# Kernel tuning notes

Hardware: AMD Instinct MI355X
Metric: run time of the kernel (lower is better)

## Reference

```python
import jax, jax.numpy as jnp
import numpy as np

B_, N, C, NH, NW = 2048, 64, 512, 16, 64  # N == window_size

def setup_inputs() -> dict:
    key = jax.random.key(0)
    k0, k1, k2, k3 = jax.random.split(key, 4)
    std = 0.02
    return {
        "inputs": jax.random.normal(k0, (B_, N, C), jnp.float32),
        "mask": jnp.zeros((NW, N, N), jnp.float32),  # (0 / -inf) additive window mask
        "qkv_w": jax.random.normal(k1, (3 * C, C), jnp.float32) * std,
        "qkv_b": jnp.zeros((3 * C,), jnp.float32),
        "proj_w": jax.random.normal(k2, (C, C), jnp.float32) * std,
        "proj_b": jnp.zeros((C,), jnp.float32),
        "bias_table": jax.random.normal(k3, (2 * N - 1, NH), jnp.float32) * std,
    }

def reference(inputs, mask, qkv_w, qkv_b, proj_w, proj_b, bias_table):
    b, n, c = inputs.shape
    nh = bias_table.shape[1]
    hd = c // nh
    scale = hd ** -0.5
    # qkv projection -> (3, B_, nh, N, hd)
    qkv = (inputs @ qkv_w.T + qkv_b).reshape(b, n, 3, nh, hd).transpose(2, 0, 3, 1, 4)
    q, k, v = qkv[0] * scale, qkv[1], qkv[2]
    attn = jnp.einsum('bhqd,bhkd->bhqk', q, k)  # (B_, nh, N, N)
    # 1D relative position bias, gathered from table
    rel_idx = jnp.arange(n)[:, None] - jnp.arange(n)[None, :] + (n - 1)  # (N, N)
    rel_bias = bias_table[rel_idx]                 # (N, N, nh)
    attn = attn + rel_bias.transpose(2, 0, 1)[None]  # add (nh, N, N)
    # additive window mask
    nw = mask.shape[0]
    attn = attn.reshape(b // nw, nw, nh, n, n) + mask[None, :, None]
    attn = jax.nn.softmax(attn.reshape(b, nh, n, n), axis=-1)
    out = jnp.einsum('bhqk,bhkd->bqhd', attn, v).reshape(b, n, c)
    return out @ proj_w.T + proj_b
```

## Files before the change

kernel.cpp:

```cpp
#include <hip/hip_runtime.h>

typedef __bf16 bf16x8 __attribute__((ext_vector_type(8)));
typedef float f32x4 __attribute__((ext_vector_type(4)));

__device__ __forceinline__ unsigned short f2bf(float x) {
  union { float f; unsigned int u; } c; c.f = x;
  unsigned int r = c.u + 0x7FFFu + ((c.u >> 16) & 1u);
  return (unsigned short)(r >> 16);
}

__global__ __launch_bounds__(256) void f32_to_bf16_vec4(
    const float* __restrict__ in, unsigned short* __restrict__ out, int n4) {
  int i = blockIdx.x * blockDim.x + threadIdx.x;
  int stride = gridDim.x * blockDim.x;
  const float4* in4 = (const float4*)in;
  ushort4* out4 = (ushort4*)out;
  for (; i < n4; i += stride) {
    float4 f = in4[i];
    ushort4 u;
    u.x = f2bf(f.x); u.y = f2bf(f.y); u.z = f2bf(f.z); u.w = f2bf(f.w);
    out4[i] = u;
  }
}

__global__ __launch_bounds__(256) void build_bias_mask(
    const float* __restrict__ bias_table,
    const float* __restrict__ mask,
    float* __restrict__ M) {
  const int idx = blockIdx.x * 256 + threadIdx.x;
  const int k = idx & 63, q = (idx >> 6) & 63, h = (idx >> 12) & 15, w = idx >> 16;
  M[idx] = bias_table[(q - k + 63) * 16 + h] + mask[(w * 64 + q) * 64 + k];
}

#define GLOAD_LDS16(gp, lp)                                                          \
  __builtin_amdgcn_global_load_lds(                                                  \
      (const __attribute__((address_space(1))) unsigned int*)(uintptr_t)(gp),        \
      (__attribute__((address_space(3))) unsigned int*)(uintptr_t)(lp), 16, 0, 0)

template <int NBN, int EPI>
__global__ __launch_bounds__(512, 2) void gemm256(
    const unsigned short* __restrict__ A,
    const unsigned short* __restrict__ B,
    const float* __restrict__ bias,
    void* __restrict__ C0, void* __restrict__ C1, void* __restrict__ C2,
    int ldc) {
  constexpr int K = 512;
  constexpr int NT = K / 64;
  __shared__ __attribute__((aligned(128))) char lds[131072];

  const int t = threadIdx.x;
  const int lane = t & 63;
  const int wid = t >> 6;
  const int wr = wid >> 2, wc = wid & 3;
  const int lr = lane & 15, lg = lane >> 4;

  const int nwg = gridDim.x;
  const int cpx = nwg >> 3;
  const int wgid = (blockIdx.x & 7) * cpx + (blockIdx.x >> 3);
  const int bm = wgid / NBN, bn = wgid % NBN;
  const int m0 = bm * 256, n0 = bn * 256;

  const char* Ab = (const char*)(A + (size_t)m0 * K);
  const char* Bb = (const char*)(B + (size_t)n0 * K);

  const int r3 = t >> 3, ps = t & 7;

  unsigned aoff[2][2], boff[2][2], adst[2][2], bdst[2][2];
#pragma unroll
  for (int j = 0; j < 2; ++j)
#pragma unroll
    for (int i = 0; i < 2; ++i) {
      const int rowA = i * 128 + j * 64 + r3;
      aoff[j][i] = (unsigned)((rowA * K + ((ps ^ (rowA & 7)) << 3)) * 2);
      adst[j][i] = (unsigned)(rowA * 128 + ps * 16);
      const int rowB = i * 128 + ((r3 >> 5) << 6) + j * 32 + (r3 & 31);
      boff[j][i] = (unsigned)((rowB * K + ((ps ^ (rowB & 7)) << 3)) * 2);
      bdst[j][i] = (unsigned)(65536 + rowB * 128 + ps * 16);
    }

#define STAGE_A(j, tt, buf)                                                   \
  do {                                                                        \
    GLOAD_LDS16(Ab + aoff[j][0] + (tt)*128, lds + (buf)*32768 + adst[j][0]);  \
    GLOAD_LDS16(Ab + aoff[j][1] + (tt)*128, lds + (buf)*32768 + adst[j][1]);  \
  } while (0)
#define STAGE_B(j, tt, buf)                                                   \
  do {                                                                        \
    GLOAD_LDS16(Bb + boff[j][0] + (tt)*128, lds + (buf)*32768 + bdst[j][0]);  \
    GLOAD_LDS16(Bb + boff[j][1] + (tt)*128, lds + (buf)*32768 + bdst[j][1]);  \
  } while (0)

  unsigned abase[2], bbase[2];
#pragma unroll
  for (int kk = 0; kk < 2; ++kk) {
    abase[kk] = (unsigned)((wr * 128 + lr) * 128 + (((kk * 4 + lg) ^ (lr & 7)) << 4));
    bbase[kk] = (unsigned)(65536 + (wc * 64 + lr) * 128 + (((kk * 4 + lg) ^ (lr & 7)) << 4));
  }

  f32x4 acc[8][4];
#pragma unroll
  for (int i = 0; i < 8; ++i)
#pragma unroll
    for (int j = 0; j < 4; ++j) acc[i][j] = f32x4{0.f, 0.f, 0.f, 0.f};

#define PHASE(QM, QN, BUF, STAGE_STMT, TAIL_STMT)                                            \
  do {                                                                                       \
    bf16x8 af[4][2], bfr[2][2];                                                              \
    _Pragma("unroll") for (int mt = 0; mt < 4; ++mt)                                         \
      _Pragma("unroll") for (int kk = 0; kk < 2; ++kk)                                       \
        af[mt][kk] = *(const bf16x8*)(lds + (BUF)*32768 + abase[kk] + (QM)*8192 + mt * 2048);\
    _Pragma("unroll") for (int nt = 0; nt < 2; ++nt)                                         \
      _Pragma("unroll") for (int kk = 0; kk < 2; ++kk)                                       \
        bfr[nt][kk] = *(const bf16x8*)(lds + (BUF)*32768 + bbase[kk] + (QN)*4096 + nt * 2048);\
    STAGE_STMT;                                                                              \
    __builtin_amdgcn_s_barrier();                                                            \
    asm volatile("s_waitcnt lgkmcnt(0)" ::: "memory");                                       \
    __builtin_amdgcn_sched_barrier(0);                                                       \
    __builtin_amdgcn_s_setprio(1);                                                           \
    _Pragma("unroll") for (int mt = 0; mt < 4; ++mt)                                         \
      _Pragma("unroll") for (int nt = 0; nt < 2; ++nt)                                       \
        _Pragma("unroll") for (int kk = 0; kk < 2; ++kk)                                     \
          acc[(QM)*4 + mt][(QN)*2 + nt] = __builtin_amdgcn_mfma_f32_16x16x32_bf16(           \
              af[mt][kk], bfr[nt][kk], acc[(QM)*4 + mt][(QN)*2 + nt], 0, 0, 0);              \
    __builtin_amdgcn_s_setprio(0);                                                           \
    TAIL_STMT;                                                                               \
    __builtin_amdgcn_s_barrier();                                                            \
  } while (0)

  STAGE_A(0, 0, 0); STAGE_B(0, 0, 0); STAGE_A(1, 0, 0); STAGE_B(1, 0, 0);
  STAGE_B(0, 1, 1); STAGE_A(1, 1, 1);
  asm volatile("s_waitcnt vmcnt(4)" ::: "memory");
  __builtin_amdgcn_s_barrier();

#pragma unroll
  for (int tt = 0; tt < NT; ++tt) {
    const int b = tt & 1;
    const int b1 = b ^ 1;
    PHASE(0, 0, b, if (tt + 1 < NT) STAGE_A(0, tt + 1, b1), (void)0);
    PHASE(1, 0, b, if (tt + 1 < NT) STAGE_B(1, tt + 1, b1), (void)0);
    PHASE(1, 1, b, if (tt + 2 < NT) STAGE_B(0, tt + 2, b), (void)0);
    if (tt + 2 < NT) {
      PHASE(0, 1, b, STAGE_A(1, tt + 2, b),
            asm volatile("s_waitcnt vmcnt(4)" ::: "memory"));
    } else if (tt + 1 < NT) {
      PHASE(0, 1, b, (void)0, asm volatile("s_waitcnt vmcnt(0)" ::: "memory"));
    } else {
      PHASE(0, 1, b, (void)0, (void)0);
    }
  }
#undef PHASE
#undef STAGE_A
#undef STAGE_B

#pragma unroll
  for (int qm = 0; qm < 2; ++qm)
#pragma unroll
    for (int mt = 0; mt < 4; ++mt)
#pragma unroll
      for (int qn = 0; qn < 2; ++qn)
#pragma unroll
        for (int nt = 0; nt < 2; ++nt) {
          const int n = n0 + wc * 64 + qn * 32 + nt * 16 + lr;
          const float bv = bias[n];
          const f32x4 a4 = acc[qm * 4 + mt][qn * 2 + nt];
          if constexpr (EPI == 2) {
            const int part = n >> 9;
            unsigned short* dst = part == 0 ? (unsigned short*)C0
                                 : (part == 1 ? (unsigned short*)C1 : (unsigned short*)C2);
            const float sc = (part == 0) ? 0.17677669529663687f : 1.0f;
            const int hh = (n >> 5) & 15, dd = n & 31;
#pragma unroll
            for (int r = 0; r < 4; ++r) {
              const int m = m0 + wr * 128 + qm * 64 + mt * 16 + lg * 4 + r;
              dst[((size_t)((m >> 6) * 16 + hh) * 64 + (m & 63)) * 32 + dd] =
                  f2bf((a4[r] + bv) * sc);
            }
          } else {
#pragma unroll
            for (int r = 0; r < 4; ++r) {
              const int m = m0 + wr * 128 + qm * 64 + mt * 16 + lg * 4 + r;
              ((float*)C0)[(size_t)m * ldc + n] = a4[r] + bv;
            }
          }
        }
}

__global__ __launch_bounds__(128) void attn_kernel(
    const unsigned short* __restrict__ Qh,
    const unsigned short* __restrict__ Kh,
    const unsigned short* __restrict__ Vh,
    const float* __restrict__ M,
    unsigned short* __restrict__ attn_out
) {
  const int wv = threadIdx.x >> 6;
  const int bh = blockIdx.x * 2 + wv;
  const int b = bh >> 4, h = bh & 15;
  const int lane = threadIdx.x & 63;
  const int lr = lane & 15, lg = lane >> 4;

  __shared__ unsigned short VtS[2][32 * 72];
  __shared__ unsigned short PlS[2][16 * 72];
  unsigned short* Vt = VtS[wv];
  unsigned short* Pl = PlS[wv];

  const unsigned short* qb = Qh + (size_t)bh * 2048;
  const unsigned short* kb = Kh + (size_t)bh * 2048;
  const unsigned short* vg = Vh + (size_t)bh * 2048;

  bf16x8 vr[4];
#pragma unroll
  for (int i = 0; i < 4; ++i) vr[i] = ((const bf16x8*)(vg + lane * 32))[i];
  bf16x8 kf[4], qf[4];
#pragma unroll
  for (int nt = 0; nt < 4; ++nt)
    kf[nt] = *(const bf16x8*)(kb + (nt * 16 + lr) * 32 + lg * 8);
#pragma unroll
  for (int mt = 0; mt < 4; ++mt)
    qf[mt] = *(const bf16x8*)(qb + (mt * 16 + lr) * 32 + lg * 8);

  {
    __bf16* vt = (__bf16*)Vt;
#pragma unroll
    for (int d = 0; d < 8; ++d) {
      vt[(d)*72 + lane] = vr[0][d];
      vt[(d + 8) * 72 + lane] = vr[1][d];
      vt[(d + 16) * 72 + lane] = vr[2][d];
      vt[(d + 24) * 72 + lane] = vr[3][d];
    }
  }
  bf16x8 vfrag[2][2];
#pragma unroll
  for (int dt = 0; dt < 2; ++dt)
#pragma unroll
    for (int ki = 0; ki < 2; ++ki)
      vfrag[dt][ki] = *(const bf16x8*)(Vt + (dt * 16 + lr) * 72 + ki * 32 + lg * 8);

  const float* Mb = M + (size_t)((b & 63) * 16 + h) * 4096;

  f32x4 o[4][2];
#pragma unroll
  for (int i = 0; i < 4; ++i)
#pragma unroll
    for (int j = 0; j < 2; ++j) o[i][j] = f32x4{0.f, 0.f, 0.f, 0.f};
  float rinv[4][4];

#pragma unroll
  for (int mt = 0; mt < 4; ++mt) {
    float mv[4][4];
#pragma unroll
    for (int r = 0; r < 4; ++r)
#pragma unroll
      for (int nt = 0; nt < 4; ++nt)
        mv[r][nt] = Mb[(mt * 16 + lg * 4 + r) * 64 + nt * 16 + lr];

    f32x4 s[4];
#pragma unroll
    for (int nt = 0; nt < 4; ++nt) s[nt] = f32x4{0.f, 0.f, 0.f, 0.f};
#pragma unroll
    for (int nt = 0; nt < 4; ++nt)
      s[nt] = __builtin_amdgcn_mfma_f32_16x16x32_bf16(qf[mt], kf[nt], s[nt], 0, 0, 0);

#pragma unroll
    for (int r = 0; r < 4; ++r) {
      float v[4];
#pragma unroll
      for (int nt = 0; nt < 4; ++nt) v[nt] = s[nt][r] + mv[r][nt];
      float mx = fmaxf(fmaxf(v[0], v[1]), fmaxf(v[2], v[3]));
      mx = fmaxf(mx, __shfl_xor(mx, 1, 64));
      mx = fmaxf(mx, __shfl_xor(mx, 2, 64));
      mx = fmaxf(mx, __shfl_xor(mx, 4, 64));
      mx = fmaxf(mx, __shfl_xor(mx, 8, 64));
      float sum = 0.f;
#pragma unroll
      for (int nt = 0; nt < 4; ++nt) {
        v[nt] = __expf(v[nt] - mx);
        sum += v[nt];
      }
      sum += __shfl_xor(sum, 1, 64);
      sum += __shfl_xor(sum, 2, 64);
      sum += __shfl_xor(sum, 4, 64);
      sum += __shfl_xor(sum, 8, 64);
      rinv[mt][r] = __builtin_amdgcn_rcpf(sum);
#pragma unroll
      for (int nt = 0; nt < 4; ++nt)
        Pl[(lg * 4 + r) * 72 + nt * 16 + lr] = f2bf(v[nt]);
    }

    bf16x8 pa[2];
#pragma unroll
    for (int ki = 0; ki < 2; ++ki)
      pa[ki] = *(const bf16x8*)(Pl + lr * 72 + ki * 32 + lg * 8);
#pragma unroll
    for (int dt = 0; dt < 2; ++dt)
#pragma unroll
      for (int ki = 0; ki < 2; ++ki)
        o[mt][dt] = __builtin_amdgcn_mfma_f32_16x16x32_bf16(pa[ki], vfrag[dt][ki], o[mt][dt], 0, 0, 0);
  }

#pragma unroll
  for (int mt = 0; mt < 4; ++mt) {
#pragma unroll
    for (int r = 0; r < 4; ++r) {
      const int m = mt * 16 + lg * 4 + r;
      const float ri = rinv[mt][r];
#pragma unroll
      for (int dt = 0; dt < 2; ++dt) {
        const int d = dt * 16 + lr;
        attn_out[(size_t)(b * 64 + m) * 512 + h * 32 + d] = f2bf(o[mt][dt][r] * ri);
      }
    }
  }
}

extern "C" void kernel_launch(void* const* d_in, const int* in_sizes, int n_in,
                              void* d_out, int out_size, void* d_ws, size_t ws_size,
                              hipStream_t stream) {
  const float* X = (const float*)d_in[0];
  const float* mask = (const float*)d_in[1];
  const float* qkv_w = (const float*)d_in[2];
  const float* qkv_b = (const float*)d_in[3];
  const float* proj_w = (const float*)d_in[4];
  const float* proj_b = (const float*)d_in[5];
  const float* bias_table = (const float*)d_in[6];
  float* out = (float*)d_out;
  char* ws = (char*)d_ws;

  unsigned short* Xb      = (unsigned short*)(ws);
  unsigned short* Qh      = (unsigned short*)(ws + 134217728ull);
  unsigned short* Kh      = (unsigned short*)(ws + 268435456ull);
  unsigned short* Vh      = (unsigned short*)(ws + 402653184ull);
  unsigned short* attnout = (unsigned short*)(ws + 536870912ull);
  unsigned short* qkv_wb  = (unsigned short*)(ws + 671088640ull);
  unsigned short* proj_wb = (unsigned short*)(ws + 672661504ull);
  float*          Mf      = (float*)(ws + 673185792ull);

  f32_to_bf16_vec4<<<2048, 256, 0, stream>>>(X, Xb, 67108864 / 4);
  f32_to_bf16_vec4<<<768, 256, 0, stream>>>(qkv_w, qkv_wb, 786432 / 4);
  f32_to_bf16_vec4<<<256, 256, 0, stream>>>(proj_w, proj_wb, 262144 / 4);
  build_bias_mask<<<16384, 256, 0, stream>>>(bias_table, mask, Mf);

  gemm256<6, 2><<<3072, 512, 0, stream>>>(Xb, qkv_wb, qkv_b, (void*)Qh, (void*)Kh, (void*)Vh, 1536);

  attn_kernel<<<16384, 128, 0, stream>>>(Qh, Kh, Vh, Mf, attnout);

  gemm256<2, 0><<<1024, 512, 0, stream>>>(attnout, proj_wb, proj_b, (void*)out, nullptr, nullptr, 512);
}
```

Before: 606.8 us.

## Switch GEMM to 32x32x16 MFMA tiles with reworked LDS staging schedule

Replaces the 16x16x32 bf16 MFMA inner loop in the 256x256 GEMM with 32x32x16 MFMAs, so each wave keeps 4x2 accumulator tiles of 16 floats. B fragments are loaded once per k-tile and reused across four M phases, and the A/B staging order and vmcnt waits are reorganised around those phases. The goal is fewer LDS fragment reads per FLOP and higher MFMA throughput. The epilogue changes to the 32x32 output layout, which gives a different store pattern that may coalesce less well, and fragment reuse may raise register pressure.

```diff
diff --git a/kernel.cpp b/kernel.cpp
--- a/kernel.cpp
+++ b/kernel.cpp
@@ -2,6 +2,7 @@
 
 typedef __bf16 bf16x8 __attribute__((ext_vector_type(8)));
 typedef float f32x4 __attribute__((ext_vector_type(4)));
+typedef float f32x16 __attribute__((ext_vector_type(16)));
 
 __device__ __forceinline__ unsigned short f2bf(float x) {
   union { float f; unsigned int u; } c; c.f = x;
@@ -52,7 +53,7 @@
   const int lane = t & 63;
   const int wid = t >> 6;
   const int wr = wid >> 2, wc = wid & 3;
-  const int lr = lane & 15, lg = lane >> 4;
+  const int l31 = lane & 31, hi = lane >> 5;
 
   const int nwg = gridDim.x;
   const int cpx = nwg >> 3;
@@ -89,99 +90,106 @@
     GLOAD_LDS16(Bb + boff[j][1] + (tt)*128, lds + (buf)*32768 + bdst[j][1]);  \
   } while (0)
 
-  unsigned abase[2], bbase[2];
-#pragma unroll
-  for (int kk = 0; kk < 2; ++kk) {
-    abase[kk] = (unsigned)((wr * 128 + lr) * 128 + (((kk * 4 + lg) ^ (lr & 7)) << 4));
-    bbase[kk] = (unsigned)(65536 + (wc * 64 + lr) * 128 + (((kk * 4 + lg) ^ (lr & 7)) << 4));
-  }
-
-  f32x4 acc[8][4];
-#pragma unroll
-  for (int i = 0; i < 8; ++i)
-#pragma unroll
-    for (int j = 0; j < 4; ++j) acc[i][j] = f32x4{0.f, 0.f, 0.f, 0.f};
-
-#define PHASE(QM, QN, BUF, STAGE_STMT, TAIL_STMT)                                            \
-  do {                                                                                       \
-    bf16x8 af[4][2], bfr[2][2];                                                              \
-    _Pragma("unroll") for (int mt = 0; mt < 4; ++mt)                                         \
-      _Pragma("unroll") for (int kk = 0; kk < 2; ++kk)                                       \
-        af[mt][kk] = *(const bf16x8*)(lds + (BUF)*32768 + abase[kk] + (QM)*8192 + mt * 2048);\
-    _Pragma("unroll") for (int nt = 0; nt < 2; ++nt)                                         \
-      _Pragma("unroll") for (int kk = 0; kk < 2; ++kk)                                       \
-        bfr[nt][kk] = *(const bf16x8*)(lds + (BUF)*32768 + bbase[kk] + (QN)*4096 + nt * 2048);\
-    STAGE_STMT;                                                                              \
-    __builtin_amdgcn_s_barrier();                                                            \
-    asm volatile("s_waitcnt lgkmcnt(0)" ::: "memory");                                       \
-    __builtin_amdgcn_sched_barrier(0);                                                       \
-    __builtin_amdgcn_s_setprio(1);                                                           \
-    _Pragma("unroll") for (int mt = 0; mt < 4; ++mt)                                         \
-      _Pragma("unroll") for (int nt = 0; nt < 2; ++nt)                                       \
-        _Pragma("unroll") for (int kk = 0; kk < 2; ++kk)                                     \
-          acc[(QM)*4 + mt][(QN)*2 + nt] = __builtin_amdgcn_mfma_f32_16x16x32_bf16(           \
-              af[mt][kk], bfr[nt][kk], acc[(QM)*4 + mt][(QN)*2 + nt], 0, 0, 0);              \
-    __builtin_amdgcn_s_setprio(0);                                                           \
-    TAIL_STMT;                                                                               \
-    __builtin_amdgcn_s_barrier();                                                            \
+  unsigned abase[4], bbase[4];
+#pragma unroll
+  for (int kk = 0; kk < 4; ++kk) {
+    const unsigned swz = (unsigned)((((kk * 2 + hi) ^ (lane & 7)) << 4));
+    abase[kk] = (unsigned)((wr * 128 + l31) * 128) + swz;
+    bbase[kk] = (unsigned)(65536 + (wc * 64 + l31) * 128) + swz;
+  }
+
+  f32x16 acc[4][2];
+#pragma unroll
+  for (int i = 0; i < 4; ++i)
+#pragma unroll
+    for (int j = 0; j < 2; ++j)
+#pragma unroll
+      for (int r = 0; r < 16; ++r) acc[i][j][r] = 0.f;
+
+#define PHASEM(MT, BUF, PRE_STMT, STAGE_STMT, TAIL_STMT)                          \
+  do {                                                                            \
+    bf16x8 af[4];                                                                 \
+    PRE_STMT;                                                                     \
+    _Pragma("unroll") for (int kk = 0; kk < 4; ++kk)                              \
+      af[kk] = *(const bf16x8*)(lds + (BUF)*32768 + abase[kk] + (MT)*4096);       \
+    STAGE_STMT;                                                                   \
+    __builtin_amdgcn_s_barrier();                                                 \
+    asm volatile("s_waitcnt lgkmcnt(0)" ::: "memory");                            \
+    __builtin_amdgcn_sched_barrier(0);                                            \
+    __builtin_amdgcn_s_setprio(1);                                                \
+    _Pragma("unroll") for (int kk = 0; kk < 4; ++kk)                              \
+      acc[MT][0] = __builtin_amdgcn_mfma_f32_32x32x16_bf16(af[kk], bf0[kk],       \
+                                                           acc[MT][0], 0, 0, 0); \
+    _Pragma("unroll") for (int kk = 0; kk < 4; ++kk)                              \
+      acc[MT][1] = __builtin_amdgcn_mfma_f32_32x32x16_bf16(af[kk], bf1[kk],       \
+                                                           acc[MT][1], 0, 0, 0); \
+    __builtin_amdgcn_s_setprio(0);                                                \
+    TAIL_STMT;                                                                    \
+    __builtin_amdgcn_s_barrier();                                                 \
   } while (0)
 
-  STAGE_A(0, 0, 0); STAGE_B(0, 0, 0); STAGE_A(1, 0, 0); STAGE_B(1, 0, 0);
-  STAGE_B(0, 1, 1); STAGE_A(1, 1, 1);
-  asm volatile("s_waitcnt vmcnt(4)" ::: "memory");
+  STAGE_A(0, 0, 0); STAGE_A(1, 0, 0); STAGE_B(0, 0, 0); STAGE_B(1, 0, 0);
+  STAGE_B(0, 1, 1); STAGE_B(1, 1, 1); STAGE_A(0, 1, 1);
+  asm volatile("s_waitcnt vmcnt(6)" ::: "memory");
   __builtin_amdgcn_s_barrier();
 
 #pragma unroll
   for (int tt = 0; tt < NT; ++tt) {
-    const int b = tt & 1;
-    const int b1 = b ^ 1;
-    PHASE(0, 0, b, if (tt + 1 < NT) STAGE_A(0, tt + 1, b1), (void)0);
-    PHASE(1, 0, b, if (tt + 1 < NT) STAGE_B(1, tt + 1, b1), (void)0);
-    PHASE(1, 1, b, if (tt + 2 < NT) STAGE_B(0, tt + 2, b), (void)0);
+    const int buf = tt & 1;
+    const int nb = buf ^ 1;
+    bf16x8 bf0[4], bf1[4];
+    PHASEM(0, buf,
+           {
+             _Pragma("unroll") for (int kk = 0; kk < 4; ++kk) {
+               bf0[kk] = *(const bf16x8*)(lds + buf * 32768 + bbase[kk]);
+               bf1[kk] = *(const bf16x8*)(lds + buf * 32768 + bbase[kk] + 4096);
+             }
+           },
+           if (tt + 1 < NT) STAGE_A(1, tt + 1, nb), (void)0);
+    PHASEM(1, buf, (void)0, if (tt + 2 < NT) STAGE_B(0, tt + 2, buf), (void)0);
+    PHASEM(2, buf, (void)0, if (tt + 2 < NT) STAGE_B(1, tt + 2, buf), (void)0);
     if (tt + 2 < NT) {
-      PHASE(0, 1, b, STAGE_A(1, tt + 2, b),
-            asm volatile("s_waitcnt vmcnt(4)" ::: "memory"));
+      PHASEM(3, buf, (void)0, STAGE_A(0, tt + 2, buf),
+             asm volatile("s_waitcnt vmcnt(6)" ::: "memory"));
     } else if (tt + 1 < NT) {
-      PHASE(0, 1, b, (void)0, asm volatile("s_waitcnt vmcnt(0)" ::: "memory"));
+      PHASEM(3, buf, (void)0, (void)0,
+             asm volatile("s_waitcnt vmcnt(0)" ::: "memory"));
     } else {
-      PHASE(0, 1, b, (void)0, (void)0);
-    }
-  }
-#undef PHASE
+      PHASEM(3, buf, (void)0, (void)0, (void)0);
+    }
+  }
+#undef PHASEM
 #undef STAGE_A
 #undef STAGE_B
 
 #pragma unroll
-  for (int qm = 0; qm < 2; ++qm)
-#pragma unroll
-    for (int mt = 0; mt < 4; ++mt)
-#pragma unroll
-      for (int qn = 0; qn < 2; ++qn)
-#pragma unroll
-        for (int nt = 0; nt < 2; ++nt) {
-          const int n = n0 + wc * 64 + qn * 32 + nt * 16 + lr;
-          const float bv = bias[n];
-          const f32x4 a4 = acc[qm * 4 + mt][qn * 2 + nt];
-          if constexpr (EPI == 2) {
-            const int part = n >> 9;
-            unsigned short* dst = part == 0 ? (unsigned short*)C0
-                                 : (part == 1 ? (unsigned short*)C1 : (unsigned short*)C2);
-            const float sc = (part == 0) ? 0.17677669529663687f : 1.0f;
-            const int hh = (n >> 5) & 15, dd = n & 31;
-#pragma unroll
-            for (int r = 0; r < 4; ++r) {
-              const int m = m0 + wr * 128 + qm * 64 + mt * 16 + lg * 4 + r;
-              dst[((size_t)((m >> 6) * 16 + hh) * 64 + (m & 63)) * 32 + dd] =
-                  f2bf((a4[r] + bv) * sc);
-            }
-          } else {
-#pragma unroll
-            for (int r = 0; r < 4; ++r) {
-              const int m = m0 + wr * 128 + qm * 64 + mt * 16 + lg * 4 + r;
-              ((float*)C0)[(size_t)m * ldc + n] = a4[r] + bv;
-            }
-          }
+  for (int mt = 0; mt < 4; ++mt) {
+#pragma unroll
+    for (int nt = 0; nt < 2; ++nt) {
+      const int n = n0 + wc * 64 + nt * 32 + l31;
+      const float bv = bias[n];
+      const f32x16 a16 = acc[mt][nt];
+      if constexpr (EPI == 2) {
+        const int part = n >> 9;
+        unsigned short* dst = part == 0 ? (unsigned short*)C0
+                               : (part == 1 ? (unsigned short*)C1 : (unsigned short*)C2);
+        const float sc = (part == 0) ? 0.17677669529663687f : 1.0f;
+        const int hh = (n >> 5) & 15, dd = n & 31;
+#pragma unroll
+        for (int r = 0; r < 16; ++r) {
+          const int m = m0 + wr * 128 + mt * 32 + (r & 3) + 8 * (r >> 2) + 4 * hi;
+          dst[((size_t)((m >> 6) * 16 + hh) * 64 + (m & 63)) * 32 + dd] =
+              f2bf((a16[r] + bv) * sc);
         }
+      } else {
+#pragma unroll
+        for (int r = 0; r < 16; ++r) {
+          const int m = m0 + wr * 128 + mt * 32 + (r & 3) + 8 * (r >> 2) + 4 * hi;
+          ((float*)C0)[(size_t)m * ldc + n] = a16[r] + bv;
+        }
+      }
+    }
+  }
 }
 
 __global__ __launch_bounds__(128) void attn_kernel(
```

After: 596.0 us. About the same (-1.8%).

## Restructure GEMM main loop into four phases that reuse A and B fragment registers

Applied to the files above, without the earlier changes.

The four-phase GEMM K-loop is reorganized. A fragments for one M-half are loaded once and reused across both N-halves, and B fragments for all four N-tiles are held in registers. This cuts LDS reads per iteration, though it needs more registers. The order of global-to-LDS staging and the vmcnt wait counts are rearranged to fit the new phase order, and the epilogue indexing is adjusted to the flattened N-tile layout.

```diff
diff --git a/kernel.cpp b/kernel.cpp
--- a/kernel.cpp
+++ b/kernel.cpp
@@ -102,52 +102,78 @@
 #pragma unroll
     for (int j = 0; j < 4; ++j) acc[i][j] = f32x4{0.f, 0.f, 0.f, 0.f};
 
-#define PHASE(QM, QN, BUF, STAGE_STMT, TAIL_STMT)                                            \
-  do {                                                                                       \
-    bf16x8 af[4][2], bfr[2][2];                                                              \
-    _Pragma("unroll") for (int mt = 0; mt < 4; ++mt)                                         \
-      _Pragma("unroll") for (int kk = 0; kk < 2; ++kk)                                       \
-        af[mt][kk] = *(const bf16x8*)(lds + (BUF)*32768 + abase[kk] + (QM)*8192 + mt * 2048);\
-    _Pragma("unroll") for (int nt = 0; nt < 2; ++nt)                                         \
-      _Pragma("unroll") for (int kk = 0; kk < 2; ++kk)                                       \
-        bfr[nt][kk] = *(const bf16x8*)(lds + (BUF)*32768 + bbase[kk] + (QN)*4096 + nt * 2048);\
-    STAGE_STMT;                                                                              \
-    __builtin_amdgcn_s_barrier();                                                            \
-    asm volatile("s_waitcnt lgkmcnt(0)" ::: "memory");                                       \
-    __builtin_amdgcn_sched_barrier(0);                                                       \
-    __builtin_amdgcn_s_setprio(1);                                                           \
-    _Pragma("unroll") for (int mt = 0; mt < 4; ++mt)                                         \
-      _Pragma("unroll") for (int nt = 0; nt < 2; ++nt)                                       \
-        _Pragma("unroll") for (int kk = 0; kk < 2; ++kk)                                     \
-          acc[(QM)*4 + mt][(QN)*2 + nt] = __builtin_amdgcn_mfma_f32_16x16x32_bf16(           \
-              af[mt][kk], bfr[nt][kk], acc[(QM)*4 + mt][(QN)*2 + nt], 0, 0, 0);              \
-    __builtin_amdgcn_s_setprio(0);                                                           \
-    TAIL_STMT;                                                                               \
-    __builtin_amdgcn_s_barrier();                                                            \
-  } while (0)
-
-  STAGE_A(0, 0, 0); STAGE_B(0, 0, 0); STAGE_A(1, 0, 0); STAGE_B(1, 0, 0);
-  STAGE_B(0, 1, 1); STAGE_A(1, 1, 1);
-  asm volatile("s_waitcnt vmcnt(4)" ::: "memory");
+#define BAR_IN()                                         \
+  __builtin_amdgcn_s_barrier();                          \
+  asm volatile("s_waitcnt lgkmcnt(0)" ::: "memory");     \
+  __builtin_amdgcn_sched_barrier(0);                     \
+  __builtin_amdgcn_s_setprio(1)
+#define MFMA16(QM, NTLO)                                                            \
+  _Pragma("unroll") for (int mt = 0; mt < 4; ++mt)                                  \
+    _Pragma("unroll") for (int nt = 0; nt < 2; ++nt)                                \
+      _Pragma("unroll") for (int kk = 0; kk < 2; ++kk)                              \
+        acc[(QM)*4 + mt][(NTLO) + nt] = __builtin_amdgcn_mfma_f32_16x16x32_bf16(    \
+            af[mt][kk], bfr[(NTLO) + nt][kk], acc[(QM)*4 + mt][(NTLO) + nt], 0, 0, 0)
+
+  STAGE_A(0, 0, 0); STAGE_B(0, 0, 0); STAGE_B(1, 0, 0); STAGE_A(1, 0, 0);
+  STAGE_A(0, 1, 1); STAGE_B(0, 1, 1);
+  asm volatile("s_waitcnt vmcnt(8)" ::: "memory");
   __builtin_amdgcn_s_barrier();
 
 #pragma unroll
   for (int tt = 0; tt < NT; ++tt) {
-    const int b = tt & 1;
-    const int b1 = b ^ 1;
-    PHASE(0, 0, b, if (tt + 1 < NT) STAGE_A(0, tt + 1, b1), (void)0);
-    PHASE(1, 0, b, if (tt + 1 < NT) STAGE_B(1, tt + 1, b1), (void)0);
-    PHASE(1, 1, b, if (tt + 2 < NT) STAGE_B(0, tt + 2, b), (void)0);
-    if (tt + 2 < NT) {
-      PHASE(0, 1, b, STAGE_A(1, tt + 2, b),
-            asm volatile("s_waitcnt vmcnt(4)" ::: "memory"));
-    } else if (tt + 1 < NT) {
-      PHASE(0, 1, b, (void)0, asm volatile("s_waitcnt vmcnt(0)" ::: "memory"));
-    } else {
-      PHASE(0, 1, b, (void)0, (void)0);
-    }
-  }
-#undef PHASE
+    const int buf = tt & 1;
+    const int nb = buf ^ 1;
+    bf16x8 af[4][2], bfr[4][2];
+#pragma unroll
+    for (int nt = 0; nt < 2; ++nt)
+#pragma unroll
+      for (int kk = 0; kk < 2; ++kk)
+        bfr[nt][kk] = *(const bf16x8*)(lds + buf * 32768 + bbase[kk] + nt * 2048);
+#pragma unroll
+    for (int mt = 0; mt < 4; ++mt)
+#pragma unroll
+      for (int kk = 0; kk < 2; ++kk)
+        af[mt][kk] = *(const bf16x8*)(lds + buf * 32768 + abase[kk] + mt * 2048);
+    if (tt + 1 < NT) STAGE_B(1, tt + 1, nb);
+    BAR_IN();
+    MFMA16(0, 0);
+    __builtin_amdgcn_s_setprio(0);
+    if (tt == NT - 1) asm volatile("s_waitcnt vmcnt(2)" ::: "memory");
+    else              asm volatile("s_waitcnt vmcnt(8)" ::: "memory");
+    __builtin_amdgcn_s_barrier();
+#pragma unroll
+    for (int nt = 2; nt < 4; ++nt)
+#pragma unroll
+      for (int kk = 0; kk < 2; ++kk)
+        bfr[nt][kk] = *(const bf16x8*)(lds + buf * 32768 + bbase[kk] + nt * 2048);
+    if (tt + 1 < NT) STAGE_A(1, tt + 1, nb);
+    BAR_IN();
+    MFMA16(0, 2);
+    __builtin_amdgcn_s_setprio(0);
+    if (tt == NT - 1) asm volatile("s_waitcnt vmcnt(0)" ::: "memory");
+    else              asm volatile("s_waitcnt vmcnt(8)" ::: "memory");
+    __builtin_amdgcn_s_barrier();
+#pragma unroll
+    for (int mt = 0; mt < 4; ++mt)
+#pragma unroll
+      for (int kk = 0; kk < 2; ++kk)
+        af[mt][kk] = *(const bf16x8*)(lds + buf * 32768 + abase[kk] + 8192 + mt * 2048);
+    if (tt + 2 < NT) STAGE_A(0, tt + 2, buf);
+    BAR_IN();
+    MFMA16(1, 0);
+    __builtin_amdgcn_s_setprio(0);
+    if (tt < NT - 1) asm volatile("s_waitcnt vmcnt(8)" ::: "memory");
+    __builtin_amdgcn_s_barrier();
+    if (tt + 2 < NT) STAGE_B(0, tt + 2, buf);
+    BAR_IN();
+    MFMA16(1, 2);
+    __builtin_amdgcn_s_setprio(0);
+    if (tt < NT - 2)       asm volatile("s_waitcnt vmcnt(8)" ::: "memory");
+    else if (tt == NT - 2) asm volatile("s_waitcnt vmcnt(4)" ::: "memory");
+    __builtin_amdgcn_s_barrier();
+  }
+#undef MFMA16
+#undef BAR_IN
 #undef STAGE_A
 #undef STAGE_B
 
@@ -156,32 +182,30 @@
 #pragma unroll
     for (int mt = 0; mt < 4; ++mt)
 #pragma unroll
-      for (int qn = 0; qn < 2; ++qn)
-#pragma unroll
-        for (int nt = 0; nt < 2; ++nt) {
-          const int n = n0 + wc * 64 + qn * 32 + nt * 16 + lr;
-          const float bv = bias[n];
-          const f32x4 a4 = acc[qm * 4 + mt][qn * 2 + nt];
-          if constexpr (EPI == 2) {
-            const int part = n >> 9;
-            unsigned short* dst = part == 0 ? (unsigned short*)C0
+      for (int nt = 0; nt < 4; ++nt) {
+        const int n = n0 + wc * 64 + nt * 16 + lr;
+        const float bv = bias[n];
+        const f32x4 a4 = acc[qm * 4 + mt][nt];
+        if constexpr (EPI == 2) {
+          const int part = n >> 9;
+          unsigned short* dst = part == 0 ? (unsigned short*)C0
                                  : (part == 1 ? (unsigned short*)C1 : (unsigned short*)C2);
-            const float sc = (part == 0) ? 0.17677669529663687f : 1.0f;
-            const int hh = (n >> 5) & 15, dd = n & 31;
-#pragma unroll
-            for (int r = 0; r < 4; ++r) {
-              const int m = m0 + wr * 128 + qm * 64 + mt * 16 + lg * 4 + r;
-              dst[((size_t)((m >> 6) * 16 + hh) * 64 + (m & 63)) * 32 + dd] =
-                  f2bf((a4[r] + bv) * sc);
-            }
-          } else {
-#pragma unroll
-            for (int r = 0; r < 4; ++r) {
-              const int m = m0 + wr * 128 + qm * 64 + mt * 16 + lg * 4 + r;
-              ((float*)C0)[(size_t)m * ldc + n] = a4[r] + bv;
-            }
+          const float sc = (part == 0) ? 0.17677669529663687f : 1.0f;
+          const int hh = (n >> 5) & 15, dd = n & 31;
+#pragma unroll
+          for (int r = 0; r < 4; ++r) {
+            const int m = m0 + wr * 128 + qm * 64 + mt * 16 + lg * 4 + r;
+            dst[((size_t)((m >> 6) * 16 + hh) * 64 + (m & 63)) * 32 + dd] =
+                f2bf((a4[r] + bv) * sc);
+          }
+        } else {
+#pragma unroll
+          for (int r = 0; r < 4; ++r) {
+            const int m = m0 + wr * 128 + qm * 64 + mt * 16 + lg * 4 + r;
+            ((float*)C0)[(size_t)m * ldc + n] = a4[r] + bv;
           }
         }
+      }
 }
 
 __global__ __launch_bounds__(128) void attn_kernel(
```

After: 579.9 us. 4.4% less time.
